# Kernel optimization log

Measured on AMD Instinct MI355X. Metric: run time of the kernel, lower is better.

The kernel has to match this reference:

```python
import jax, jax.numpy as jnp
import numpy as np

B, N, M = 4, 4096, 1024
QUERY_DIM, CONTEXT_DIM = 1024, 768
HEADS, DIM_HEAD = 16, 64
INNER = HEADS * DIM_HEAD  # 1024


def setup_inputs() -> dict:
    key = jax.random.key(0)
    ks = jax.random.split(key, 7)
    s_q = 1.0 / np.sqrt(QUERY_DIM)
    s_c = 1.0 / np.sqrt(CONTEXT_DIM)
    s_i = 1.0 / np.sqrt(INNER)
    return {
        "x": jax.random.normal(ks[0], (B, N, QUERY_DIM), dtype=jnp.float32),
        "context": jax.random.normal(ks[1], (B, M, CONTEXT_DIM), dtype=jnp.float32),
        # weights stored [in, out] so y = x @ W (equiv to torch Linear with W.T)
        "Wq": jax.random.uniform(ks[2], (QUERY_DIM, INNER), minval=-s_q, maxval=s_q, dtype=jnp.float32),
        "Wk": jax.random.uniform(ks[3], (CONTEXT_DIM, INNER), minval=-s_c, maxval=s_c, dtype=jnp.float32),
        "Wv": jax.random.uniform(ks[4], (CONTEXT_DIM, INNER), minval=-s_c, maxval=s_c, dtype=jnp.float32),
        "Wo": jax.random.uniform(ks[5], (INNER, QUERY_DIM), minval=-s_i, maxval=s_i, dtype=jnp.float32),
        "bo": jax.random.uniform(ks[6], (QUERY_DIM,), minval=-s_i, maxval=s_i, dtype=jnp.float32),
    }


def reference(x, context, Wq, Wk, Wv, Wo, bo):
    scale = DIM_HEAD ** -0.5
    b, n, _ = x.shape
    m = context.shape[1]
    # projections, then split heads: [B, H, S, Dh]
    q = (x @ Wq).reshape(b, n, HEADS, DIM_HEAD).transpose(0, 2, 1, 3)
    k = (context @ Wk).reshape(b, m, HEADS, DIM_HEAD).transpose(0, 2, 1, 3)
    v = (context @ Wv).reshape(b, m, HEADS, DIM_HEAD).transpose(0, 2, 1, 3)
    sim = jnp.einsum('bhid,bhjd->bhij', q, k) * scale  # [B,H,N,M]
    attn = jax.nn.softmax(sim, axis=-1)
    out = jnp.einsum('bhij,bhjd->bhid', attn, v)       # [B,H,N,Dh]
    out = out.transpose(0, 2, 1, 3).reshape(b, n, INNER)
    return out @ Wo + bo
```

## Files before the change

kernel.cpp:

```cpp
#include <hip/hip_runtime.h>
#include <hip/hip_bf16.h>

typedef unsigned short u16;
typedef __attribute__((ext_vector_type(8))) short short8;
typedef __attribute__((ext_vector_type(4))) float f32x4;
typedef __attribute__((ext_vector_type(16))) float f32x16;
typedef __attribute__((ext_vector_type(2))) unsigned uint2v;

#define ATT_B 4
#define ATT_N 4096
#define ATT_M 1024
#define ATT_H 16
#define CBLK 64
#define NT (ATT_M / CBLK)

__device__ inline u16 f2bf(float f) {
  union { float f; unsigned u; } x; x.f = f;
  unsigned r = x.u + 0x7fffu + ((x.u >> 16) & 1u);
  return (u16)(r >> 16);
}

__device__ inline unsigned pk_bf16(float lo, float hi) {
  unsigned r;
  asm("v_cvt_pk_bf16_f32 %0, %1, %2" : "=v"(r) : "v"(lo), "v"(hi));
  return r;
}

__device__ inline float exp2_raw(float x) {
  float r;
  asm("v_exp_f32 %0, %1" : "=v"(r) : "v"(x));
  return r;
}

__device__ inline void gload_lds16(const u16* g, u16* l) {
  __builtin_amdgcn_global_load_lds(
      (const __attribute__((address_space(1))) void*)g,
      (__attribute__((address_space(3))) void*)l, 16, 0, 0);
}

__global__ __launch_bounds__(256) void prep_kernel(
    const float* __restrict__ x, u16* __restrict__ xb, int n4x,
    const float* __restrict__ ctx, u16* __restrict__ cb, int n4c,
    const float* __restrict__ Wq, const float* __restrict__ Wk,
    const float* __restrict__ Wv, const float* __restrict__ Wo,
    u16* __restrict__ wqt, u16* __restrict__ wkt,
    u16* __restrict__ wvt, u16* __restrict__ wot) {
  const int blk = blockIdx.x;
  const int tid = threadIdx.x;
  if (blk < 4096) {
    const int z = blk >> 10;
    const float* W = (z == 0) ? Wq : (z == 1) ? Wk : (z == 2) ? Wv : Wo;
    u16* Wt = (z == 0) ? wqt : (z == 1) ? wkt : (z == 2) ? wvt : wot;
    const int K = (z == 0 || z == 3) ? 1024 : 768;
    const int k0 = ((blk >> 5) & 31) * 32;
    if (k0 >= K) return;
    const int n0 = (blk & 31) * 32;
    __shared__ float T[32][33];
    const int tx = tid & 31, ty = tid >> 5;
#pragma unroll
    for (int i = 0; i < 4; ++i)
      T[ty + i * 8][tx] = W[(size_t)(k0 + ty + i * 8) * 1024 + n0 + tx];
    __syncthreads();
#pragma unroll
    for (int i = 0; i < 4; ++i)
      Wt[(size_t)(n0 + ty + i * 8) * K + k0 + tx] = f2bf(T[tx][ty + i * 8]);
  } else {
    int i = (blk - 4096) * 256 + tid;
    const float* src;
    u16* dst;
    if (i < n4x) {
      src = x; dst = xb;
    } else {
      i -= n4x;
      if (i >= n4c) return;
      src = ctx; dst = cb;
    }
    const float4 v = reinterpret_cast<const float4*>(src)[i];
    uint2 o;
    o.x = pk_bf16(v.x, v.y);
    o.y = pk_bf16(v.z, v.w);
    reinterpret_cast<uint2*>(dst)[i] = o;
  }
}

template <int F32OUT>
__device__ __forceinline__ void gemm_body(const u16* __restrict__ A,
                                          const u16* __restrict__ Bt,
                                          u16* __restrict__ Cb,
                                          float* __restrict__ Cf,
                                          const float* __restrict__ bias,
                                          float scale, int N, int K,
                                          unsigned orig, unsigned gx, unsigned nwg,
                                          u16* As, u16* Bs) {
  const int tid = threadIdx.x;
  const int lane = tid & 63;
  const int w = tid >> 6;
  const int lr = lane & 15;
  const int lk = lane >> 4;
  const int wm = w >> 1, wn = w & 1;

  const unsigned cpx = nwg >> 3;
  const unsigned swz = (orig & 7u) * cpx + (orig >> 3);
  const int brow = (int)(swz / gx) * 128;
  const int bcol = (int)(swz % gx) * 128;

  const int gr = lane >> 3;
  const int gc = (lane & 7) ^ gr;

  f32x4 acc[4][4];
#pragma unroll
  for (int mi = 0; mi < 4; ++mi)
#pragma unroll
    for (int ni = 0; ni < 4; ++ni) acc[mi][ni] = f32x4{0.f, 0.f, 0.f, 0.f};

  for (int k0 = 0; k0 < K; k0 += 64) {
#pragma unroll
    for (int i = 0; i < 4; ++i) {
      const int g = w * 4 + i;
      gload_lds16(A + (size_t)(brow + g * 8 + gr) * K + k0 + gc * 8, &As[g * 512]);
      gload_lds16(Bt + (size_t)(bcol + g * 8 + gr) * K + k0 + gc * 8, &Bs[g * 512]);
    }
    __syncthreads();
    short8 a[4][2], bb[4][2];
#pragma unroll
    for (int mi = 0; mi < 4; ++mi) {
      const int row = wm * 64 + mi * 16 + lr;
#pragma unroll
      for (int kk = 0; kk < 2; ++kk)
        a[mi][kk] = *reinterpret_cast<const short8*>(
            &As[row * 64 + (((kk * 4 + lk) ^ (lr & 7)) * 8)]);
    }
#pragma unroll
    for (int ni = 0; ni < 4; ++ni) {
      const int row = wn * 64 + ni * 16 + lr;
#pragma unroll
      for (int kk = 0; kk < 2; ++kk)
        bb[ni][kk] = *reinterpret_cast<const short8*>(
            &Bs[row * 64 + (((kk * 4 + lk) ^ (lr & 7)) * 8)]);
    }
#pragma unroll
    for (int mi = 0; mi < 4; ++mi)
#pragma unroll
      for (int ni = 0; ni < 4; ++ni)
#pragma unroll
        for (int kk = 0; kk < 2; ++kk)
          acc[mi][ni] = __builtin_amdgcn_mfma_f32_16x16x32_bf16(
              a[mi][kk], bb[ni][kk], acc[mi][ni], 0, 0, 0);
    __syncthreads();
  }

#pragma unroll
  for (int mi = 0; mi < 4; ++mi)
#pragma unroll
    for (int ni = 0; ni < 4; ++ni)
#pragma unroll
      for (int r = 0; r < 4; ++r) {
        const size_t row = (size_t)(brow + wm * 64 + mi * 16 + lk * 4 + r);
        const int col = bcol + wn * 64 + ni * 16 + lr;
        if (F32OUT)
          Cf[row * N + col] = acc[mi][ni][r] + bias[col];
        else
          Cb[row * N + col] = f2bf(acc[mi][ni][r] * scale);
      }
}

__global__ __launch_bounds__(256) void proj3(
    const u16* __restrict__ xb, const u16* __restrict__ wqt, u16* __restrict__ Qb,
    float qscale,
    const u16* __restrict__ cb, const u16* __restrict__ wkt, u16* __restrict__ Kb,
    const u16* __restrict__ wvt, u16* __restrict__ VTb) {
  __shared__ u16 As[128 * 64];
  __shared__ u16 Bs[128 * 64];
  const unsigned blk = blockIdx.x;
  if (blk < 1024)
    gemm_body<0>(xb, wqt, Qb, nullptr, nullptr, qscale, 1024, 1024,
                 blk, 8u, 1024u, As, Bs);
  else if (blk < 1280)
    gemm_body<0>(cb, wkt, Kb, nullptr, nullptr, 1.0f, 1024, 768,
                 blk - 1024u, 8u, 256u, As, Bs);
  else
    gemm_body<0>(wvt, cb, VTb, nullptr, nullptr, 1.0f, 4096, 768,
                 blk - 1280u, 32u, 256u, As, Bs);
}

template <int F32OUT>
__global__ __launch_bounds__(256) void gemm_bt(const u16* __restrict__ A,
                                               const u16* __restrict__ Bt,
                                               u16* __restrict__ Cb,
                                               float* __restrict__ Cf,
                                               const float* __restrict__ bias,
                                               float scale, int N, int K) {
  __shared__ u16 As[128 * 64];
  __shared__ u16 Bs[128 * 64];
  const unsigned gx = gridDim.x;
  const unsigned nwg = gx * gridDim.y;
  const unsigned orig = blockIdx.y * gx + blockIdx.x;
  gemm_body<F32OUT>(A, Bt, Cb, Cf, bias, scale, N, K, orig, gx, nwg, As, Bs);
}

__global__ __launch_bounds__(512, 4) void attn_kernel(const u16* __restrict__ Qg,
                                                      const u16* __restrict__ Kg,
                                                      const u16* __restrict__ VTg,
                                                      u16* __restrict__ AO) {
  __shared__ u16 Ks[2][8][512];
  __shared__ u16 Vs[2][8][512];
  __shared__ float lsw[8][32];

  const int tid = threadIdx.x;
  const int lane = tid & 63;
  const int w = tid >> 6;
  const int l = lane & 31;
  const int hi = lane >> 5;
  const int qt = blockIdx.x;
  const int bh = blockIdx.y;
  const int b = bh >> 4, h = bh & 15;
  const int qbase = qt * 256 + w * 32;

  short8 qf[4];
#pragma unroll
  for (int kc = 0; kc < 4; ++kc)
    qf[kc] = *reinterpret_cast<const short8*>(
        Qg + (size_t)(b * ATT_N + qbase + l) * 1024 + h * 64 + kc * 16 + hi * 8);

  const u16* ksrc = Kg + (size_t)(b * ATT_M + (w >> 2) * 32 + l) * 1024 + h * 64 + (w & 3) * 16 + hi * 8;
  const u16* vsrc = VTg + (size_t)(h * 64 + (w >> 2) * 32 + l) * (ATT_B * ATT_M) + b * ATT_M + (w & 3) * 16 + hi * 8;

  f32x16 Oacc[2];
  float lsum = 0.f;
#pragma unroll
  for (int r = 0; r < 16; ++r) { Oacc[0][r] = 0.f; Oacc[1][r] = 0.f; }

  gload_lds16(ksrc, &Ks[0][w][0]);
  gload_lds16(vsrc, &Vs[0][w][0]);
  __syncthreads();

  int buf = 0;
  for (int t = 0; t < NT; ++t) {
    if (t + 1 < NT) {
      gload_lds16(ksrc + (size_t)(t + 1) * CBLK * 1024, &Ks[buf ^ 1][w][0]);
      gload_lds16(vsrc + (size_t)(t + 1) * CBLK, &Vs[buf ^ 1][w][0]);
    }

    f32x16 st[2];
#pragma unroll
    for (int r = 0; r < 16; ++r) { st[0][r] = 0.f; st[1][r] = 0.f; }
    __builtin_amdgcn_s_setprio(1);
#pragma unroll
    for (int ci = 0; ci < 2; ++ci)
#pragma unroll
      for (int kc = 0; kc < 4; ++kc) {
        short8 kb = *reinterpret_cast<const short8*>(&Ks[buf][ci * 4 + kc][lane * 8]);
        st[ci] = __builtin_amdgcn_mfma_f32_32x32x16_bf16(kb, qf[kc], st[ci], 0, 0, 0);
      }
    __builtin_amdgcn_s_setprio(0);

    short8 pa[4];
#pragma unroll
    for (int ci = 0; ci < 2; ++ci) {
      float p[16];
      float s = 0.f;
#pragma unroll
      for (int r = 0; r < 16; ++r) { p[r] = exp2_raw(st[ci][r]); s += p[r]; }
      lsum += s;
      unsigned Y0 = pk_bf16(p[0], p[1]),   Y1 = pk_bf16(p[2], p[3]);
      unsigned Y2 = pk_bf16(p[4], p[5]),   Y3 = pk_bf16(p[6], p[7]);
      unsigned Y4 = pk_bf16(p[8], p[9]),   Y5 = pk_bf16(p[10], p[11]);
      unsigned Y6 = pk_bf16(p[12], p[13]), Y7 = pk_bf16(p[14], p[15]);
      uint2v s02 = __builtin_amdgcn_permlane32_swap(Y0, Y2, false, false);
      uint2v s13 = __builtin_amdgcn_permlane32_swap(Y1, Y3, false, false);
      uint2v s46 = __builtin_amdgcn_permlane32_swap(Y4, Y6, false, false);
      uint2v s57 = __builtin_amdgcn_permlane32_swap(Y5, Y7, false, false);
      union { unsigned u[4]; short8 s; } f0, f1;
      f0.u[0] = s02.x; f0.u[1] = s13.x; f0.u[2] = s02.y; f0.u[3] = s13.y;
      f1.u[0] = s46.x; f1.u[1] = s57.x; f1.u[2] = s46.y; f1.u[3] = s57.y;
      pa[ci * 2 + 0] = f0.s;
      pa[ci * 2 + 1] = f1.s;
    }

    __builtin_amdgcn_s_setprio(1);
#pragma unroll
    for (int kcc = 0; kcc < 4; ++kcc)
#pragma unroll
      for (int dj = 0; dj < 2; ++dj) {
        short8 vb = *reinterpret_cast<const short8*>(&Vs[buf][dj * 4 + kcc][lane * 8]);
        Oacc[dj] = __builtin_amdgcn_mfma_f32_32x32x16_bf16(pa[kcc], vb, Oacc[dj], 0, 0, 0);
      }
    __builtin_amdgcn_s_setprio(0);

    __syncthreads();
    buf ^= 1;
  }

  lsum += __shfl_xor(lsum, 32);
  if (hi == 0) lsw[w][l] = lsum;
  __syncthreads();
#pragma unroll
  for (int r = 0; r < 16; ++r) {
    const int crow = (r & 3) + 8 * (r >> 2) + 4 * hi;
    const float inv = __builtin_amdgcn_rcpf(lsw[w][crow]);
    const size_t row = (size_t)(b * ATT_N + qbase + crow);
#pragma unroll
    for (int dj = 0; dj < 2; ++dj)
      AO[row * 1024 + h * 64 + dj * 32 + l] = f2bf(Oacc[dj][r] * inv);
  }
}

extern "C" void kernel_launch(void* const* d_in, const int* in_sizes, int n_in,
                              void* d_out, int out_size, void* d_ws, size_t ws_size,
                              hipStream_t stream) {
  const float* x   = (const float*)d_in[0];
  const float* ctx = (const float*)d_in[1];
  const float* Wq  = (const float*)d_in[2];
  const float* Wk  = (const float*)d_in[3];
  const float* Wv  = (const float*)d_in[4];
  const float* Wo  = (const float*)d_in[5];
  const float* bo  = (const float*)d_in[6];
  float* out = (float*)d_out;

  char* ws = (char*)d_ws;
  u16* xb  = (u16*)(ws);
  u16* cb  = (u16*)(ws + 33554432);
  u16* wqt = (u16*)(ws + 39845888);
  u16* wkt = (u16*)(ws + 41943040);
  u16* wvt = (u16*)(ws + 43515904);
  u16* wot = (u16*)(ws + 45088768);
  u16* Qb  = (u16*)(ws + 47185920);
  u16* Kb  = (u16*)(ws + 80740352);
  u16* VTb = (u16*)(ws + 89128960);
  u16* AOb = xb;

  prep_kernel<<<23552, 256, 0, stream>>>(x, xb, 4194304, ctx, cb, 786432,
                                         Wq, Wk, Wv, Wo, wqt, wkt, wvt, wot);

  const float qscale = 0.125f * 1.44269504088896f;
  proj3<<<1536, 256, 0, stream>>>(xb, wqt, Qb, qscale, cb, wkt, Kb, wvt, VTb);

  attn_kernel<<<dim3(16, 64), 512, 0, stream>>>(Qb, Kb, VTb, AOb);

  gemm_bt<1><<<dim3(8, 128), 256, 0, stream>>>(AOb, wot, nullptr, out, bo, 1.0f, 1024, 1024);
}
```

Baseline: 209.6 us.

## Use 256x256-tile double-buffered 8-wave GEMM for Q and output projections

```diff
diff --git a/kernel.cpp b/kernel.cpp
--- a/kernel.cpp
+++ b/kernel.cpp
@@ -164,38 +164,145 @@
       }
 }
 
-__global__ __launch_bounds__(256) void proj3(
-    const u16* __restrict__ xb, const u16* __restrict__ wqt, u16* __restrict__ Qb,
-    float qscale,
+__global__ __launch_bounds__(256) void proj_kv(
     const u16* __restrict__ cb, const u16* __restrict__ wkt, u16* __restrict__ Kb,
     const u16* __restrict__ wvt, u16* __restrict__ VTb) {
   __shared__ u16 As[128 * 64];
   __shared__ u16 Bs[128 * 64];
   const unsigned blk = blockIdx.x;
-  if (blk < 1024)
-    gemm_body<0>(xb, wqt, Qb, nullptr, nullptr, qscale, 1024, 1024,
-                 blk, 8u, 1024u, As, Bs);
-  else if (blk < 1280)
+  if (blk < 256)
     gemm_body<0>(cb, wkt, Kb, nullptr, nullptr, 1.0f, 1024, 768,
-                 blk - 1024u, 8u, 256u, As, Bs);
+                 blk, 8u, 256u, As, Bs);
   else
     gemm_body<0>(wvt, cb, VTb, nullptr, nullptr, 1.0f, 4096, 768,
-                 blk - 1280u, 32u, 256u, As, Bs);
+                 blk - 256u, 32u, 256u, As, Bs);
 }
 
 template <int F32OUT>
-__global__ __launch_bounds__(256) void gemm_bt(const u16* __restrict__ A,
-                                               const u16* __restrict__ Bt,
-                                               u16* __restrict__ Cb,
-                                               float* __restrict__ Cf,
-                                               const float* __restrict__ bias,
-                                               float scale, int N, int K) {
-  __shared__ u16 As[128 * 64];
-  __shared__ u16 Bs[128 * 64];
+__global__ __launch_bounds__(512, 2) void gemm8(const u16* __restrict__ A,
+                                                const u16* __restrict__ Bt,
+                                                u16* __restrict__ Cb,
+                                                float* __restrict__ Cf,
+                                                const float* __restrict__ bias,
+                                                float scale, int N, int K) {
+  __shared__ u16 As[2][16384];
+  __shared__ u16 Bs[2][16384];
+  const int tid = threadIdx.x;
+  const int lane = tid & 63;
+  const int w = tid >> 6;
+  const int lr = lane & 15;
+  const int lk = lane >> 4;
+  const int wm = w >> 2, wn = w & 3;
+  const int gr = lane >> 3;
+  const int gc = (lane & 7) ^ gr;
+
   const unsigned gx = gridDim.x;
   const unsigned nwg = gx * gridDim.y;
   const unsigned orig = blockIdx.y * gx + blockIdx.x;
-  gemm_body<F32OUT>(A, Bt, Cb, Cf, bias, scale, N, K, orig, gx, nwg, As, Bs);
+  const unsigned cpx = nwg >> 3;
+  const unsigned swz = (orig & 7u) * cpx + (orig >> 3);
+  const int brow = (int)(swz / gx) * 256;
+  const int bcol = (int)(swz % gx) * 256;
+
+  int ag[2][2];
+#pragma unroll
+  for (int p = 0; p < 2; ++p)
+#pragma unroll
+    for (int j = 0; j < 2; ++j) {
+      const int i = 2 * w + j;
+      const int q = 2 * p + (i >> 3);
+      const int wi = i & 7;
+      ag[p][j] = (wi < 4) ? (4 * q + wi) : (16 + 4 * q + (wi - 4));
+    }
+
+#define G8_SA(d, kt, g) \
+  gload_lds16(A + (size_t)(brow + (g) * 8 + gr) * K + (kt) * 64 + gc * 8, &As[d][(g) * 512])
+#define G8_SB(d, kt, g) \
+  gload_lds16(Bt + (size_t)(bcol + (g) * 8 + gr) * K + (kt) * 64 + gc * 8, &Bs[d][(g) * 512])
+
+  f32x4 acc[8][4];
+#pragma unroll
+  for (int m = 0; m < 8; ++m)
+#pragma unroll
+    for (int n = 0; n < 4; ++n) acc[m][n] = f32x4{0.f, 0.f, 0.f, 0.f};
+
+  const int NKT = K >> 6;
+
+  G8_SB(0, 0, 4 * w + 0); G8_SB(0, 0, 4 * w + 1);
+  G8_SB(0, 0, 4 * w + 2); G8_SB(0, 0, 4 * w + 3);
+  G8_SA(0, 0, ag[0][0]); G8_SA(0, 0, ag[0][1]);
+  G8_SA(0, 0, ag[1][0]); G8_SA(0, 0, ag[1][1]);
+
+  for (int t = 0; t < NKT; ++t) {
+    const int cur = t & 1, nxt = cur ^ 1;
+    const bool pf = (t + 1) < NKT;
+    const int kt1 = t + 1;
+    short8 bfr[4][2];
+#pragma unroll
+    for (int q = 0; q < 4; ++q) {
+      if (q == 0) {
+        asm volatile("s_waitcnt vmcnt(2)" ::: "memory");
+        __builtin_amdgcn_s_barrier();
+        asm volatile("" ::: "memory");
+      } else if (q == 2) {
+        if (pf) asm volatile("s_waitcnt vmcnt(4)" ::: "memory");
+        else    asm volatile("s_waitcnt vmcnt(0)" ::: "memory");
+        __builtin_amdgcn_s_barrier();
+        asm volatile("" ::: "memory");
+      }
+      short8 afr[2][2];
+#pragma unroll
+      for (int j = 0; j < 2; ++j) {
+        const int row = wm * 128 + (2 * q + j) * 16 + lr;
+#pragma unroll
+        for (int kk = 0; kk < 2; ++kk)
+          afr[j][kk] = *reinterpret_cast<const short8*>(
+              &As[cur][row * 64 + (((kk * 4 + lk) ^ (lr & 7)) * 8)]);
+      }
+      if (q == 0) {
+#pragma unroll
+        for (int n = 0; n < 4; ++n) {
+          const int row = wn * 64 + n * 16 + lr;
+#pragma unroll
+          for (int kk = 0; kk < 2; ++kk)
+            bfr[n][kk] = *reinterpret_cast<const short8*>(
+                &Bs[cur][row * 64 + (((kk * 4 + lk) ^ (lr & 7)) * 8)]);
+        }
+      }
+      if (pf) {
+        if (q == 0)      { G8_SB(nxt, kt1, 4 * w + 0); G8_SB(nxt, kt1, 4 * w + 1); }
+        else if (q == 1) { G8_SB(nxt, kt1, 4 * w + 2); G8_SB(nxt, kt1, 4 * w + 3); }
+        else if (q == 2) { G8_SA(nxt, kt1, ag[0][0]);  G8_SA(nxt, kt1, ag[0][1]); }
+        else             { G8_SA(nxt, kt1, ag[1][0]);  G8_SA(nxt, kt1, ag[1][1]); }
+      }
+      __builtin_amdgcn_s_setprio(1);
+#pragma unroll
+      for (int j = 0; j < 2; ++j)
+#pragma unroll
+        for (int n = 0; n < 4; ++n)
+#pragma unroll
+          for (int kk = 0; kk < 2; ++kk)
+            acc[2 * q + j][n] = __builtin_amdgcn_mfma_f32_16x16x32_bf16(
+                afr[j][kk], bfr[n][kk], acc[2 * q + j][n], 0, 0, 0);
+      __builtin_amdgcn_s_setprio(0);
+    }
+  }
+#undef G8_SA
+#undef G8_SB
+
+#pragma unroll
+  for (int m = 0; m < 8; ++m)
+#pragma unroll
+    for (int n = 0; n < 4; ++n)
+#pragma unroll
+      for (int r = 0; r < 4; ++r) {
+        const size_t row = (size_t)(brow + wm * 128 + m * 16 + lk * 4 + r);
+        const int col = bcol + wn * 64 + n * 16 + lr;
+        if (F32OUT)
+          Cf[row * N + col] = acc[m][n][r] + bias[col];
+        else
+          Cb[row * N + col] = f2bf(acc[m][n][r] * scale);
+      }
 }
 
 __global__ __launch_bounds__(512, 4) void attn_kernel(const u16* __restrict__ Qg,
@@ -333,9 +440,10 @@
                                          Wq, Wk, Wv, Wo, wqt, wkt, wvt, wot);
 
   const float qscale = 0.125f * 1.44269504088896f;
-  proj3<<<1536, 256, 0, stream>>>(xb, wqt, Qb, qscale, cb, wkt, Kb, wvt, VTb);
+  gemm8<0><<<dim3(4, 64), 512, 0, stream>>>(xb, wqt, Qb, nullptr, nullptr, qscale, 1024, 1024);
+  proj_kv<<<512, 256, 0, stream>>>(cb, wkt, Kb, wvt, VTb);
 
   attn_kernel<<<dim3(16, 64), 512, 0, stream>>>(Qb, Kb, VTb, AOb);
 
-  gemm_bt<1><<<dim3(8, 128), 256, 0, stream>>>(AOb, wot, nullptr, out, bo, 1.0f, 1024, 1024);
-}
+  gemm8<1><<<dim3(4, 64), 512, 0, stream>>>(AOb, wot, nullptr, out, bo, 1.0f, 1024, 1024);
+}
```

Result: faster. 202.2 us (-3.5%).
